# Optimization experiments

Measured on AMD Instinct MI355X. Metric: run time of the kernel, lower is better.

## Reference

```python
import jax, jax.numpy as jnp
import numpy as np

V = 200000  # number of variables (fixed num_segments for aggregation)


def setup_inputs() -> dict:
    key = jax.random.key(0)
    ks = jax.random.split(key, 10)
    E, D, Fe, P = 1000000, 128, 16, 2
    Hm, Hag, Ha = 256, 256, 256  # mem_hidden, mem_agg_hidden, agg_hidden
    Din = D + Fe + 1

    def w(k, shape):
        return jax.random.normal(k, shape, jnp.float32) / jnp.sqrt(shape[1])

    return {
        "variable_state": jax.random.normal(ks[0], (E, D), jnp.float32),
        "edge_feature": jax.random.normal(ks[1], (E, Fe), jnp.float32),
        "solution": jax.random.uniform(ks[2], (V,), jnp.float32),
        "W1m": w(ks[3], (Hm, Din)), "b1m": jnp.zeros((Hm,), jnp.float32),
        "W2m": w(ks[4], (Hag, Hm)),
        "W1a": w(ks[5], (Ha, Hag)), "b1a": jnp.zeros((Ha,), jnp.float32),
        "W2a": w(ks[6], (D, Ha)),
        "Wc": w(ks[7], (P, D)), "bc": jnp.zeros((P,), jnp.float32),
        "variable_index": jax.random.randint(ks[8], (E,), 0, V, jnp.int32),
        "edge_sign": 2 * jax.random.randint(ks[9], (E,), 0, 2, jnp.int32) - 1,
    }


def reference(variable_state, edge_feature, solution, W1m, b1m, W2m, W1a, b1a,
              W2a, Wc, bc, variable_index, edge_sign):
    ls = jax.nn.log_sigmoid
    # per-edge signed solution column: mm(signed_mask, solution) on the sparse incidence
    signed = (edge_sign.astype(jnp.float32) * solution[variable_index])[:, None]  # [E,1]
    x = jnp.concatenate([variable_state, edge_feature, signed], axis=1)  # [E, Din]
    # memory MLP: Linear -> logsigmoid -> Linear -> logsigmoid
    s = ls(ls(x @ W1m.T + b1m) @ W2m.T)  # [E, Hag]
    # aggregation mm(variable_mask, state): sum edges per variable
    agg = jax.ops.segment_sum(s, variable_index, num_segments=V)  # [V, Hag]
    # aggregator MLP
    h = ls(ls(agg @ W1a.T + b1a) @ W2a.T)  # [V, D]
    # variable classifier
    return h @ Wc.T + bc  # [V, P]
```

## Files before the change

kernel.cpp:

```cpp
#include <hip/hip_runtime.h>
#include <hip/hip_bf16.h>

typedef unsigned short u16;
typedef __attribute__((ext_vector_type(8))) short   short8;
typedef __attribute__((ext_vector_type(8))) __bf16  bf16x8;
typedef __attribute__((ext_vector_type(16))) float  floatx16;

#define DD  128
#define FE  16
#define DIN 145
#define K1  160
#define K1P 168
#define HQ  256
#define HQP 264
#define ME  64
#define MV  32

#define H1IDX(r, c) ((((r) * HQ) + (c)) ^ (((r) & 7) << 3))

__device__ __forceinline__ float logsig(float x) {
    return fminf(x, 0.f) - __logf(1.f + __expf(-fabsf(x)));
}
__device__ __forceinline__ u16 f2b(float f) {
    union { float f; unsigned u; } x; x.f = f;
    unsigned r = x.u + 0x7fffu + ((x.u >> 16) & 1u);
    return (u16)(r >> 16);
}
__device__ __forceinline__ ushort4 f2b4(float4 v) {
    ushort4 o; o.x = f2b(v.x); o.y = f2b(v.y); o.z = f2b(v.z); o.w = f2b(v.w);
    return o;
}
__device__ __forceinline__ bf16x8 ld_bf8_lds(const short* p) {
    return __builtin_bit_cast(bf16x8, *(const short8*)p);
}
__device__ __forceinline__ bf16x8 ld_bf8_glb(const short* p) {
    return __builtin_bit_cast(bf16x8, *(const short8*)p);
}

__global__ __launch_bounds__(256) void conv_weights(
    const float* __restrict__ W1m, const float* __restrict__ W2m,
    const float* __restrict__ W1a, const float* __restrict__ W2a,
    short* __restrict__ W1mb, short* __restrict__ W2mb,
    short* __restrict__ W1ab, short* __restrict__ W2ab)
{
    int i = blockIdx.x * 256 + threadIdx.x;
    if (i < 256 * K1) {
        int n = i / K1, k = i - n * K1;
        W1mb[i] = (k < DIN) ? (short)f2b(W1m[n * DIN + k]) : (short)0;
    } else if (i < 256 * K1 + 256 * HQ) {
        int j = i - 256 * K1;
        W2mb[j] = (short)f2b(W2m[j]);
    } else if (i < 256 * K1 + 2 * 256 * HQ) {
        int j = i - 256 * K1 - 256 * HQ;
        W1ab[j] = (short)f2b(W1a[j]);
    } else if (i < 256 * K1 + 2 * 256 * HQ + 128 * HQ) {
        int j = i - 256 * K1 - 2 * 256 * HQ;
        W2ab[j] = (short)f2b(W2a[j]);
    }
}

__global__ __launch_bounds__(512, 6) void edge_mfma(
    const float* __restrict__ vs, const float* __restrict__ ef,
    const float* __restrict__ sol, const float* __restrict__ b1m,
    const short* __restrict__ W1mb, const short* __restrict__ W2mb,
    const int* __restrict__ vidx, const int* __restrict__ esign,
    float* __restrict__ agg, int E)
{
    __shared__ short xs[ME * K1P];
    __shared__ short h1s[ME * HQ];
    const int tid = threadIdx.x;
    const int e0 = blockIdx.x * ME;

    if (tid < ME) {
        int ge = e0 + tid;
        int v  = vidx[ge];
        *(int*)&xs[tid * K1P + 164] = v;
        xs[tid * K1P + 144] = (short)f2b((float)esign[ge] * sol[v]);
        #pragma unroll
        for (int k = 145; k < K1; ++k) xs[tid * K1P + k] = 0;
    }
    for (int i = tid; i < ME * 32; i += 512) {
        int e = i >> 5, q = (i & 31) << 2;
        float4 v = *(const float4*)&vs[(size_t)(e0 + e) * DD + q];
        *(ushort4*)&xs[e * K1P + q] = f2b4(v);
    }
    for (int i = tid; i < ME * 4; i += 512) {
        int e = i >> 2, q = (i & 3) << 2;
        float4 v = *(const float4*)&ef[(size_t)(e0 + e) * FE + q];
        *(ushort4*)&xs[e * K1P + DD + q] = f2b4(v);
    }
    __syncthreads();

    const int wv = tid >> 6, lane = tid & 63;
    const int lr = lane & 31, lh = lane >> 5;
    const int n0 = wv * 32;

    floatx16 a0 = {}, a1 = {};
    {
        const short* Wb = W1mb + (size_t)(n0 + lr) * K1;
        #pragma unroll 2
        for (int ks = 0; ks < K1 / 16; ++ks) {
            int k = ks * 16 + lh * 8;
            bf16x8 A0 = ld_bf8_lds(&xs[lr * K1P + k]);
            bf16x8 A1 = ld_bf8_lds(&xs[(32 + lr) * K1P + k]);
            bf16x8 B  = ld_bf8_glb(&Wb[k]);
            a0 = __builtin_amdgcn_mfma_f32_32x32x16_bf16(A0, B, a0, 0, 0, 0);
            a1 = __builtin_amdgcn_mfma_f32_32x32x16_bf16(A1, B, a1, 0, 0, 0);
        }
    }
    {
        float bn = b1m[n0 + lr];
        #pragma unroll
        for (int r = 0; r < 16; ++r) {
            int row = (r & 3) + 8 * (r >> 2) + 4 * lh;
            h1s[H1IDX(row,      n0 + lr)] = (short)f2b(logsig(a0[r] + bn));
            h1s[H1IDX(32 + row, n0 + lr)] = (short)f2b(logsig(a1[r] + bn));
        }
    }
    __syncthreads();

    a0 = (floatx16){}; a1 = (floatx16){};
    {
        const short* Wb = W2mb + (size_t)(n0 + lr) * HQ;
        #pragma unroll 2
        for (int ks = 0; ks < HQ / 16; ++ks) {
            int k = ks * 16 + lh * 8;
            bf16x8 A0 = ld_bf8_lds(&h1s[H1IDX(lr,      k)]);
            bf16x8 A1 = ld_bf8_lds(&h1s[H1IDX(32 + lr, k)]);
            bf16x8 B  = ld_bf8_glb(&Wb[k]);
            a0 = __builtin_amdgcn_mfma_f32_32x32x16_bf16(A0, B, a0, 0, 0, 0);
            a1 = __builtin_amdgcn_mfma_f32_32x32x16_bf16(A1, B, a1, 0, 0, 0);
        }
    }
    #pragma unroll
    for (int r = 0; r < 16; ++r) {
        int row = (r & 3) + 8 * (r >> 2) + 4 * lh;
        int va = *(const int*)&xs[row * K1P + 164];
        int vb = *(const int*)&xs[(32 + row) * K1P + 164];
        atomicAdd(&agg[(size_t)va * HQ + n0 + lr], logsig(a0[r]));
        atomicAdd(&agg[(size_t)vb * HQ + n0 + lr], logsig(a1[r]));
    }
}

__global__ __launch_bounds__(512, 6) void var_mfma(
    const float* __restrict__ agg, const float* __restrict__ b1a,
    const short* __restrict__ W1ab, const short* __restrict__ W2ab,
    const float* __restrict__ Wc, const float* __restrict__ bc,
    float* __restrict__ out, int V)
{
    __shared__ short as_s[MV][HQP];
    __shared__ short h1v[MV][HQP];
    __shared__ float hsv[MV][DD + 4];
    const int tid = threadIdx.x;
    const int v0 = blockIdx.x * MV;

    for (int i = tid; i < MV * 64; i += 512) {
        int v = i >> 6, q = (i & 63) << 2;
        float4 a = *(const float4*)&agg[(size_t)(v0 + v) * HQ + q];
        *(ushort4*)&as_s[v][q] = f2b4(a);
    }
    __syncthreads();

    const int wv = tid >> 6, lane = tid & 63;
    const int lr = lane & 31, lh = lane >> 5;
    const int n0 = wv * 32;

    floatx16 c0 = {};
    {
        const short* Wb = W1ab + (size_t)(n0 + lr) * HQ;
        #pragma unroll 2
        for (int ks = 0; ks < HQ / 16; ++ks) {
            int k = ks * 16 + lh * 8;
            bf16x8 A = ld_bf8_lds(&as_s[lr][k]);
            bf16x8 B = ld_bf8_glb(&Wb[k]);
            c0 = __builtin_amdgcn_mfma_f32_32x32x16_bf16(A, B, c0, 0, 0, 0);
        }
    }
    {
        float bn = b1a[n0 + lr];
        #pragma unroll
        for (int r = 0; r < 16; ++r) {
            int row = (r & 3) + 8 * (r >> 2) + 4 * lh;
            h1v[row][n0 + lr] = (short)f2b(logsig(c0[r] + bn));
        }
    }
    __syncthreads();

    if (wv < 4) {
        floatx16 d0 = {};
        const int n0b = wv * 32;
        const short* Wb = W2ab + (size_t)(n0b + lr) * HQ;
        #pragma unroll 2
        for (int ks = 0; ks < HQ / 16; ++ks) {
            int k = ks * 16 + lh * 8;
            bf16x8 A = ld_bf8_lds(&h1v[lr][k]);
            bf16x8 B = ld_bf8_glb(&Wb[k]);
            d0 = __builtin_amdgcn_mfma_f32_32x32x16_bf16(A, B, d0, 0, 0, 0);
        }
        #pragma unroll
        for (int r = 0; r < 16; ++r) {
            int row = (r & 3) + 8 * (r >> 2) + 4 * lh;
            hsv[row][n0b + lr] = logsig(d0[r]);
        }
    }
    __syncthreads();

    if (tid < MV * 2) {
        int v = tid >> 1, p = tid & 1;
        const float* wrow = Wc + (size_t)p * DD;
        float acc = bc[p];
        for (int k = 0; k < DD; k += 4) {
            float4 w4 = *(const float4*)&wrow[k];
            float4 h4 = *(const float4*)&hsv[v][k];
            acc = fmaf(w4.w, h4.w, fmaf(w4.z, h4.z, fmaf(w4.y, h4.y, fmaf(w4.x, h4.x, acc))));
        }
        out[(size_t)(v0 + v) * 2 + p] = acc;
    }
}

extern "C" void kernel_launch(void* const* d_in, const int* in_sizes, int n_in,
                              void* d_out, int out_size, void* d_ws, size_t ws_size,
                              hipStream_t stream) {
    const float* vs  = (const float*)d_in[0];
    const float* ef  = (const float*)d_in[1];
    const float* sol = (const float*)d_in[2];
    const float* W1m = (const float*)d_in[3];
    const float* b1m = (const float*)d_in[4];
    const float* W2m = (const float*)d_in[5];
    const float* W1a = (const float*)d_in[6];
    const float* b1a = (const float*)d_in[7];
    const float* W2a = (const float*)d_in[8];
    const float* Wc  = (const float*)d_in[9];
    const float* bc  = (const float*)d_in[10];
    const int* vidx  = (const int*)d_in[11];
    const int* sgn   = (const int*)d_in[12];

    const int E = in_sizes[0] / DD;
    const int V = in_sizes[2];

    char* ws = (char*)d_ws;
    float* agg = (float*)ws;
    size_t off = (size_t)V * HQ * sizeof(float);
    short* W1mb = (short*)(ws + off); off += (size_t)256 * K1 * 2;
    short* W2mb = (short*)(ws + off); off += (size_t)256 * HQ * 2;
    short* W1ab = (short*)(ws + off); off += (size_t)256 * HQ * 2;
    short* W2ab = (short*)(ws + off);

    hipMemsetAsync(agg, 0, (size_t)V * HQ * sizeof(float), stream);
    conv_weights<<<dim3(800), dim3(256), 0, stream>>>(
        W1m, W2m, W1a, W2a, W1mb, W2mb, W1ab, W2ab);
    edge_mfma<<<dim3(E / ME), dim3(512), 0, stream>>>(
        vs, ef, sol, b1m, W1mb, W2mb, vidx, sgn, agg, E);
    var_mfma<<<dim3(V / MV), dim3(512), 0, stream>>>(
        agg, b1a, W1ab, W2ab, Wc, bc, (float*)d_out, V);
}
```

Before: 1.657 ms.

## Pre-pack edge inputs to bf16 and double-buffer tiles in a persistent edge kernel

Adds a pass that converts the per-edge state, features, signed solution and variable index into a packed bf16 row buffer. A persistent edge kernel then streams 64-edge tiles into LDS with global_load_lds and double buffering, overlapping the next tile's load with the second GEMM. The variable kernel doubles its rows per block to 64 and reuses shared memory across stages. This adds a full extra write and read of a large packed buffer, depends on enough workspace being available, and lowers occupancy bounds.

```diff
diff --git a/kernel.cpp b/kernel.cpp
--- a/kernel.cpp
+++ b/kernel.cpp
@@ -14,9 +14,8 @@
 #define HQ  256
 #define HQP 264
 #define ME  64
-#define MV  32
-
-#define H1IDX(r, c) ((((r) * HQ) + (c)) ^ (((r) & 7) << 3))
+#define MV  64
+#define EGRID 2048
 
 __device__ __forceinline__ float logsig(float x) {
     return fminf(x, 0.f) - __logf(1.f + __expf(-fabsf(x)));
@@ -35,6 +34,11 @@
 }
 __device__ __forceinline__ bf16x8 ld_bf8_glb(const short* p) {
     return __builtin_bit_cast(bf16x8, *(const short8*)p);
+}
+__device__ __forceinline__ void load_lds16(const void* g, void* l) {
+    __builtin_amdgcn_global_load_lds(
+        (const __attribute__((address_space(1))) unsigned int*)g,
+        (__attribute__((address_space(3))) unsigned int*)l, 16, 0, 0);
 }
 
 __global__ __launch_bounds__(256) void conv_weights(
@@ -59,7 +63,119 @@
     }
 }
 
-__global__ __launch_bounds__(512, 6) void edge_mfma(
+__global__ __launch_bounds__(256) void conv_pack(
+    const float* __restrict__ vs, const float* __restrict__ ef,
+    const float* __restrict__ sol, const int* __restrict__ vidx,
+    const int* __restrict__ sgn, short* __restrict__ packed, int E)
+{
+    const int tid  = blockIdx.x * 256 + threadIdx.x;
+    const int nthr = gridDim.x * 256;
+    for (long i = tid; i < (long)E * 32; i += nthr) {
+        long e = i >> 5; int q = (int)(i & 31) << 2;
+        float4 v = *(const float4*)&vs[(size_t)e * DD + q];
+        *(ushort4*)&packed[(size_t)e * K1P + q] = f2b4(v);
+    }
+    for (long i = tid; i < (long)E * 4; i += nthr) {
+        long e = i >> 2; int q = (int)(i & 3) << 2;
+        float4 v = *(const float4*)&ef[(size_t)e * FE + q];
+        *(ushort4*)&packed[(size_t)e * K1P + DD + q] = f2b4(v);
+    }
+    for (long e = tid; e < E; e += nthr) {
+        int vI = vidx[e];
+        u16 s  = f2b((float)sgn[e] * sol[vI]);
+        int4 z0 = {(int)s, 0, 0, 0};
+        int4 z1 = {0, 0, 0, 0};
+        int4 z2 = {0, 0, vI, 0};
+        *(int4*)&packed[(size_t)e * K1P + 144] = z0;
+        *(int4*)&packed[(size_t)e * K1P + 152] = z1;
+        *(int4*)&packed[(size_t)e * K1P + 160] = z2;
+    }
+}
+
+__global__ __launch_bounds__(512, 4) void edge_mfma_staged(
+    const float* __restrict__ b1m,
+    const short* __restrict__ W1mb, const short* __restrict__ W2mb,
+    const short* __restrict__ packed, float* __restrict__ agg, int NT)
+{
+    __shared__ short xs[2][ME * K1P];
+    __shared__ short h1s[ME][HQP];
+    const int tid = threadIdx.x;
+    const int wv = tid >> 6, lane = tid & 63;
+    const int lr = lane & 31, lh = lane >> 5;
+    const int n0 = wv * 32;
+
+    int t = blockIdx.x;
+    if (t >= NT) return;
+
+    auto stage = [&](int buf, int tt) {
+        const char* src = (const char*)packed + (size_t)tt * (ME * K1P * 2);
+        char* dst = (char*)&xs[buf][0];
+        #pragma unroll
+        for (int rnd = 0; rnd < 3; ++rnd) {
+            int base = rnd * 8192 + wv * 1024;
+            if (base < ME * K1P * 2)
+                load_lds16(src + base + lane * 16, dst + base);
+        }
+    };
+
+    stage(0, t);
+    __syncthreads();
+
+    const float bn = b1m[n0 + lr];
+    const short* Wb1 = W1mb + (size_t)(n0 + lr) * K1;
+    const short* Wb2 = W2mb + (size_t)(n0 + lr) * HQ;
+
+    int i = 0;
+    while (true) {
+        const short* xsc = &xs[i & 1][0];
+
+        floatx16 a0 = {}, a1 = {};
+        #pragma unroll 2
+        for (int ks = 0; ks < K1 / 16; ++ks) {
+            int k = ks * 16 + lh * 8;
+            bf16x8 A0 = ld_bf8_lds(&xsc[lr * K1P + k]);
+            bf16x8 A1 = ld_bf8_lds(&xsc[(32 + lr) * K1P + k]);
+            bf16x8 B  = ld_bf8_glb(&Wb1[k]);
+            a0 = __builtin_amdgcn_mfma_f32_32x32x16_bf16(A0, B, a0, 0, 0, 0);
+            a1 = __builtin_amdgcn_mfma_f32_32x32x16_bf16(A1, B, a1, 0, 0, 0);
+        }
+        #pragma unroll
+        for (int r = 0; r < 16; ++r) {
+            int row = (r & 3) + 8 * (r >> 2) + 4 * lh;
+            h1s[row][n0 + lr]      = (short)f2b(logsig(a0[r] + bn));
+            h1s[32 + row][n0 + lr] = (short)f2b(logsig(a1[r] + bn));
+        }
+        __syncthreads();
+
+        int tn = t + gridDim.x;
+        if (tn < NT) stage((i + 1) & 1, tn);
+
+        a0 = (floatx16){}; a1 = (floatx16){};
+        #pragma unroll 2
+        for (int ks = 0; ks < HQ / 16; ++ks) {
+            int k = ks * 16 + lh * 8;
+            bf16x8 A0 = ld_bf8_lds(&h1s[lr][k]);
+            bf16x8 A1 = ld_bf8_lds(&h1s[32 + lr][k]);
+            bf16x8 B  = ld_bf8_glb(&Wb2[k]);
+            a0 = __builtin_amdgcn_mfma_f32_32x32x16_bf16(A0, B, a0, 0, 0, 0);
+            a1 = __builtin_amdgcn_mfma_f32_32x32x16_bf16(A1, B, a1, 0, 0, 0);
+        }
+        #pragma unroll
+        for (int r = 0; r < 16; ++r) {
+            int row = (r & 3) + 8 * (r >> 2) + 4 * lh;
+            int va = *(const int*)&xsc[row * K1P + 164];
+            int vb = *(const int*)&xsc[(32 + row) * K1P + 164];
+            atomicAdd(&agg[(size_t)va * HQ + n0 + lr], logsig(a0[r]));
+            atomicAdd(&agg[(size_t)vb * HQ + n0 + lr], logsig(a1[r]));
+        }
+        if (tn >= NT) break;
+        __syncthreads();
+        t = tn; ++i;
+    }
+}
+
+#define H1IDX(r, c) ((((r) * HQ) + (c)) ^ (((r) & 7) << 3))
+__global__ __launch_bounds__(512, 6) void edge_mfma_legacy(
     const float* __restrict__ vs, const float* __restrict__ ef,
     const float* __restrict__ sol, const float* __restrict__ b1m,
     const short* __restrict__ W1mb, const short* __restrict__ W2mb,
@@ -142,15 +258,16 @@
     }
 }
 
-__global__ __launch_bounds__(512, 6) void var_mfma(
+__global__ __launch_bounds__(512, 4) void var_mfma(
     const float* __restrict__ agg, const float* __restrict__ b1a,
     const short* __restrict__ W1ab, const short* __restrict__ W2ab,
     const float* __restrict__ Wc, const float* __restrict__ bc,
     float* __restrict__ out, int V)
 {
-    __shared__ short as_s[MV][HQP];
-    __shared__ short h1v[MV][HQP];
-    __shared__ float hsv[MV][DD + 4];
+    __shared__ short smem[2][MV * HQP];
+    short (*as_s)[HQP] = (short(*)[HQP])&smem[0][0];
+    short (*h1v)[HQP]  = (short(*)[HQP])&smem[1][0];
+    float (*hsv)[DD + 4] = (float(*)[DD + 4])&smem[0][0];
     const int tid = threadIdx.x;
     const int v0 = blockIdx.x * MV;
 
@@ -165,15 +282,17 @@
     const int lr = lane & 31, lh = lane >> 5;
     const int n0 = wv * 32;
 
-    floatx16 c0 = {};
+    floatx16 c0 = {}, c1 = {};
     {
         const short* Wb = W1ab + (size_t)(n0 + lr) * HQ;
         #pragma unroll 2
         for (int ks = 0; ks < HQ / 16; ++ks) {
             int k = ks * 16 + lh * 8;
-            bf16x8 A = ld_bf8_lds(&as_s[lr][k]);
-            bf16x8 B = ld_bf8_glb(&Wb[k]);
-            c0 = __builtin_amdgcn_mfma_f32_32x32x16_bf16(A, B, c0, 0, 0, 0);
+            bf16x8 A0 = ld_bf8_lds(&as_s[lr][k]);
+            bf16x8 A1 = ld_bf8_lds(&as_s[32 + lr][k]);
+            bf16x8 B  = ld_bf8_glb(&Wb[k]);
+            c0 = __builtin_amdgcn_mfma_f32_32x32x16_bf16(A0, B, c0, 0, 0, 0);
+            c1 = __builtin_amdgcn_mfma_f32_32x32x16_bf16(A1, B, c1, 0, 0, 0);
         }
     }
     {
@@ -181,26 +300,27 @@
         #pragma unroll
         for (int r = 0; r < 16; ++r) {
             int row = (r & 3) + 8 * (r >> 2) + 4 * lh;
-            h1v[row][n0 + lr] = (short)f2b(logsig(c0[r] + bn));
-        }
-    }
-    __syncthreads();
-
-    if (wv < 4) {
+            h1v[row][n0 + lr]      = (short)f2b(logsig(c0[r] + bn));
+            h1v[32 + row][n0 + lr] = (short)f2b(logsig(c1[r] + bn));
+        }
+    }
+    __syncthreads();
+
+    {
+        const int rh = wv >> 2, n0b = (wv & 3) * 32;
         floatx16 d0 = {};
-        const int n0b = wv * 32;
         const short* Wb = W2ab + (size_t)(n0b + lr) * HQ;
         #pragma unroll 2
         for (int ks = 0; ks < HQ / 16; ++ks) {
             int k = ks * 16 + lh * 8;
-            bf16x8 A = ld_bf8_lds(&h1v[lr][k]);
+            bf16x8 A = ld_bf8_lds(&h1v[rh * 32 + lr][k]);
             bf16x8 B = ld_bf8_glb(&Wb[k]);
             d0 = __builtin_amdgcn_mfma_f32_32x32x16_bf16(A, B, d0, 0, 0, 0);
         }
         #pragma unroll
         for (int r = 0; r < 16; ++r) {
             int row = (r & 3) + 8 * (r >> 2) + 4 * lh;
-            hsv[row][n0b + lr] = logsig(d0[r]);
+            hsv[rh * 32 + row][n0b + lr] = logsig(d0[r]);
         }
     }
     __syncthreads();
@@ -237,20 +357,36 @@
 
     const int E = in_sizes[0] / DD;
     const int V = in_sizes[2];
+    const int NT = E / ME;
 
     char* ws = (char*)d_ws;
-    float* agg = (float*)ws;
-    size_t off = (size_t)V * HQ * sizeof(float);
-    short* W1mb = (short*)(ws + off); off += (size_t)256 * K1 * 2;
-    short* W2mb = (short*)(ws + off); off += (size_t)256 * HQ * 2;
-    short* W1ab = (short*)(ws + off); off += (size_t)256 * HQ * 2;
-    short* W2ab = (short*)(ws + off);
+    size_t off = 0;
+    auto alloc = [&](size_t bytes) {
+        char* p = ws + off;
+        off = (off + bytes + 255) & ~(size_t)255;
+        return p;
+    };
+    float* agg    = (float*)alloc((size_t)V * HQ * sizeof(float));
+    short* W1mb   = (short*)alloc((size_t)256 * K1 * 2);
+    short* W2mb   = (short*)alloc((size_t)256 * HQ * 2);
+    short* W1ab   = (short*)alloc((size_t)256 * HQ * 2);
+    short* W2ab   = (short*)alloc((size_t)128 * HQ * 2);
+    short* packed = (short*)alloc((size_t)E * K1P * 2);
+    const bool use_pack = (off <= ws_size);
 
     hipMemsetAsync(agg, 0, (size_t)V * HQ * sizeof(float), stream);
     conv_weights<<<dim3(800), dim3(256), 0, stream>>>(
         W1m, W2m, W1a, W2a, W1mb, W2mb, W1ab, W2ab);
-    edge_mfma<<<dim3(E / ME), dim3(512), 0, stream>>>(
-        vs, ef, sol, b1m, W1mb, W2mb, vidx, sgn, agg, E);
+
+    if (use_pack) {
+        conv_pack<<<dim3(EGRID), dim3(256), 0, stream>>>(
+            vs, ef, sol, vidx, sgn, packed, E);
+        edge_mfma_staged<<<dim3(EGRID), dim3(512), 0, stream>>>(
+            b1m, W1mb, W2mb, packed, agg, NT);
+    } else {
+        edge_mfma_legacy<<<dim3(NT), dim3(512), 0, stream>>>(
+            vs, ef, sol, b1m, W1mb, W2mb, vidx, sgn, agg, E);
+    }
     var_mfma<<<dim3(V / MV), dim3(512), 0, stream>>>(
         agg, b1a, W1ab, W2ab, Wc, bc, (float*)d_out, V);
 }
```

After: 1.906 ms. 15.0% more time.
